# Optimization experiments

Hardware: AMD Instinct MI355X
Metric: run time of the kernel (lower is better)

## Reference

```python
import jax, jax.numpy as jnp
import numpy as np

N_VERTS = 100000  # vertices per mesh; K = 3*N_VERTS


def det3x3(m):
    # m: [..., 3, 3] closed-form determinant (cheaper than generic LU det)
    a00, a01, a02 = m[..., 0, 0], m[..., 0, 1], m[..., 0, 2]
    a10, a11, a12 = m[..., 1, 0], m[..., 1, 1], m[..., 1, 2]
    a20, a21, a22 = m[..., 2, 0], m[..., 2, 1], m[..., 2, 2]
    return (a00 * (a11 * a22 - a12 * a21)
            - a01 * (a10 * a22 - a12 * a20)
            + a02 * (a10 * a21 - a11 * a20))


def setup_inputs() -> dict:
    key = jax.random.key(0)
    k1, k2 = jax.random.split(key)
    x = jax.random.normal(k1, (64, 3 * N_VERTS), dtype=jnp.float32)
    M = jax.random.randint(k2, (200000, 3), 0, N_VERTS, dtype=jnp.int64)
    return {"x": x, "M": M}


def reference(x, M):
    B = x.shape[0]
    v = x.reshape(B, -1, 3)          # [B, N, 3]
    tets = v[:, M]                    # gather -> [B, T, 3, 3]
    vol = jnp.sum(jnp.abs(det3x3(tets)), axis=1) / 6.0  # [B]
    scale = vol ** (1.0 / 3.0)        # cube root of volume
    out = v / scale[:, None, None]    # broadcast divide
    return out.reshape(x.shape)
```

## Files before the change

### kernel.cpp

```cpp
#include <hip/hip_runtime.h>
#include <hip/hip_fp16.h>


constexpr int NV   = 100000;
constexpr int NT   = 200000;
constexpr int NB   = 64;
constexpr int ROW  = 3 * NV;
constexpr int ROW4 = ROW / 4;

typedef float vfloat4 __attribute__((ext_vector_type(4)));

__global__ __launch_bounds__(256) void transpose_kernel(
    const float* __restrict__ x, __half* __restrict__ xt, float* __restrict__ ws)
{
    __shared__ float tile[64][65];
    if (blockIdx.x == 0 && threadIdx.x < NB) ws[threadIdx.x] = 0.0f;

    const int c0 = blockIdx.x * 64;
    const int l  = threadIdx.x & 63;
    const int w  = threadIdx.x >> 6;

    const int c = c0 + l;
    if (c < ROW) {
        #pragma unroll
        for (int k = 0; k < 16; ++k) {
            const int b = w * 16 + k;
            tile[l][b] = x[(size_t)b * ROW + c];
        }
    }
    __syncthreads();

    const int b2 = (l & 31) * 2;
    #pragma unroll
    for (int k = 0; k < 8; ++k) {
        const int r  = (l >> 5) + 2 * w + 8 * k;
        const int cc = c0 + r;
        if (cc < ROW) {
            __half2 h = __floats2half2_rn(tile[r][b2], tile[r][b2 + 1]);
            *(__half2*)&xt[(size_t)cc * NB + b2] = h;
        }
    }
}

__global__ __launch_bounds__(256) void vol_reduce_kernel(
    const __half* __restrict__ xt,
    const int*    __restrict__ M,
    float*        __restrict__ ws)
{
    const int lane  = threadIdx.x & 63;
    const int wib   = threadIdx.x >> 6;
    const int wid   = blockIdx.x * 4 + wib;
    const int nw    = gridDim.x * 4;
    const int chunk = (NT + nw - 1) / nw;
    const int t0 = wid * chunk;
    const int t1 = min(NT, t0 + chunk);

    const __half* __restrict__ base = xt + lane;
    float acc = 0.0f;
    #pragma unroll 4
    for (int t = t0; t < t1; ++t) {
        const int i0 = M[3 * t + 0];
        const int i1 = M[3 * t + 1];
        const int i2 = M[3 * t + 2];
        const __half* p0 = base + (size_t)i0 * 192;
        const __half* p1 = base + (size_t)i1 * 192;
        const __half* p2 = base + (size_t)i2 * 192;
        const float a00 = __half2float(p0[0]);
        const float a01 = __half2float(p0[64]);
        const float a02 = __half2float(p0[128]);
        const float a10 = __half2float(p1[0]);
        const float a11 = __half2float(p1[64]);
        const float a12 = __half2float(p1[128]);
        const float a20 = __half2float(p2[0]);
        const float a21 = __half2float(p2[64]);
        const float a22 = __half2float(p2[128]);
        const float det = a00 * (a11 * a22 - a12 * a21)
                        - a01 * (a10 * a22 - a12 * a20)
                        + a02 * (a10 * a21 - a11 * a20);
        acc += fabsf(det);
    }

    __shared__ float sacc[4][NB];
    sacc[wib][lane] = acc;
    __syncthreads();
    if (threadIdx.x < NB)
        atomicAdd(&ws[threadIdx.x],
                  sacc[0][threadIdx.x] + sacc[1][threadIdx.x] +
                  sacc[2][threadIdx.x] + sacc[3][threadIdx.x]);
}

__global__ __launch_bounds__(256) void scale_kernel(
    const vfloat4* __restrict__ x,
    const float*   __restrict__ ws,
    vfloat4*       __restrict__ out)
{
    const int idx = blockIdx.x * 256 + threadIdx.x;
    const int b   = idx / ROW4;
    const float s = cbrtf(6.0f / ws[b]);
    vfloat4 vv = x[idx];
    vv *= s;
    __builtin_nontemporal_store(vv, &out[idx]);
}

extern "C" void kernel_launch(void* const* d_in, const int* in_sizes, int n_in,
                              void* d_out, int out_size, void* d_ws, size_t ws_size,
                              hipStream_t stream)
{
    const float* x   = (const float*)d_in[0];
    const int*   M   = (const int*)d_in[1];
    float*       out = (float*)d_out;
    float*       ws  = (float*)d_ws;
    __half*      xt  = (__half*)(ws + 256);

    transpose_kernel<<<(ROW + 63) / 64, 256, 0, stream>>>(x, xt, ws);

    vol_reduce_kernel<<<2048, 256, 0, stream>>>(xt, M, ws);

    scale_kernel<<<NB * ROW4 / 256, 256, 0, stream>>>((const vfloat4*)x, ws, (vfloat4*)out);
}
```

Baseline: 220.1 us.

## Interleave vertex xyz per batch in fp16 table and gather 12-byte vectors

The transposed fp16 table now stores each vertex as [batch][xyz] instead of [coord][batch], so one 12-byte load brings a vertex's xyz for two batches. The volume kernel splits each wave into two halves that handle two tetrahedra, and each lane handles two batches. This replaces nine scattered 2-byte gathers with three vector loads. The transpose kernel is reorganised to tile 32 vertices per block, with index div/mod arithmetic to build packed outputs. A cross-half shuffle then combines the partial sums. The cost is more integer arithmetic in the transpose and 12-byte loads that are only 4-byte aligned.

```diff
diff --git a/kernel.cpp b/kernel.cpp
--- a/kernel.cpp
+++ b/kernel.cpp
@@ -9,36 +9,43 @@
 constexpr int ROW4 = ROW / 4;
 
 typedef float vfloat4 __attribute__((ext_vector_type(4)));
+typedef unsigned int uint3v __attribute__((ext_vector_type(3)));
+
+union gpack { uint3v v; __half h[6]; };
 
 __global__ __launch_bounds__(256) void transpose_kernel(
     const float* __restrict__ x, __half* __restrict__ xt, float* __restrict__ ws)
 {
-    __shared__ float tile[64][65];
+    __shared__ float tile[96][65];
     if (blockIdx.x == 0 && threadIdx.x < NB) ws[threadIdx.x] = 0.0f;
 
-    const int c0 = blockIdx.x * 64;
-    const int l  = threadIdx.x & 63;
-    const int w  = threadIdx.x >> 6;
+    const int v0 = blockIdx.x * 32;
+    const int c0 = v0 * 3;
 
-    const int c = c0 + l;
-    if (c < ROW) {
-        #pragma unroll
-        for (int k = 0; k < 16; ++k) {
-            const int b = w * 16 + k;
-            tile[l][b] = x[(size_t)b * ROW + c];
-        }
+    #pragma unroll
+    for (int k = 0; k < 24; ++k) {
+        const int idx = threadIdx.x + k * 256;
+        const int b   = idx / 96;
+        const int cc  = idx - b * 96;
+        tile[cc][b] = x[(size_t)b * ROW + c0 + cc];
     }
     __syncthreads();
 
-    const int b2 = (l & 31) * 2;
+    uint2* outp = (uint2*)(xt + (size_t)v0 * 192);
     #pragma unroll
-    for (int k = 0; k < 8; ++k) {
-        const int r  = (l >> 5) + 2 * w + 8 * k;
-        const int cc = c0 + r;
-        if (cc < ROW) {
-            __half2 h = __floats2half2_rn(tile[r][b2], tile[r][b2 + 1]);
-            *(__half2*)&xt[(size_t)cc * NB + b2] = h;
+    for (int k = 0; k < 6; ++k) {
+        const int j = threadIdx.x + k * 256;
+        union { uint2 u; __half h[4]; } pk;
+        #pragma unroll
+        for (int i = 0; i < 4; ++i) {
+            const int o   = 4 * j + i;
+            const int dv  = o / 192;
+            const int rem = o - dv * 192;
+            const int b   = rem / 3;
+            const int c   = rem - b * 3;
+            pk.h[i] = __float2half_rn(tile[3 * dv + c][b]);
         }
+        outp[j] = pk.u;
     }
 }
 
@@ -47,41 +54,56 @@
     const int*    __restrict__ M,
     float*        __restrict__ ws)
 {
-    const int lane  = threadIdx.x & 63;
-    const int wib   = threadIdx.x >> 6;
-    const int wid   = blockIdx.x * 4 + wib;
-    const int nw    = gridDim.x * 4;
-    const int chunk = (NT + nw - 1) / nw;
-    const int t0 = wid * chunk;
-    const int t1 = min(NT, t0 + chunk);
+    const int lane = threadIdx.x & 63;
+    const int wib  = threadIdx.x >> 6;
+    const int wid  = blockIdx.x * 4 + wib;
+    const int nw   = gridDim.x * 4;
+    const int NP   = NT / 2;
+    const int chunk = (NP + nw - 1) / nw;
+    const int p0 = wid * chunk;
+    const int p1 = min(NP, p0 + chunk);
 
-    const __half* __restrict__ base = xt + lane;
-    float acc = 0.0f;
+    const int hsel = lane >> 5;
+    const int bl   = lane & 31;
+    const __half* __restrict__ base = xt + bl * 6;
+
+    float accA = 0.0f, accB = 0.0f;
     #pragma unroll 4
-    for (int t = t0; t < t1; ++t) {
-        const int i0 = M[3 * t + 0];
-        const int i1 = M[3 * t + 1];
-        const int i2 = M[3 * t + 2];
-        const __half* p0 = base + (size_t)i0 * 192;
-        const __half* p1 = base + (size_t)i1 * 192;
-        const __half* p2 = base + (size_t)i2 * 192;
-        const float a00 = __half2float(p0[0]);
-        const float a01 = __half2float(p0[64]);
-        const float a02 = __half2float(p0[128]);
-        const float a10 = __half2float(p1[0]);
-        const float a11 = __half2float(p1[64]);
-        const float a12 = __half2float(p1[128]);
-        const float a20 = __half2float(p2[0]);
-        const float a21 = __half2float(p2[64]);
-        const float a22 = __half2float(p2[128]);
-        const float det = a00 * (a11 * a22 - a12 * a21)
-                        - a01 * (a10 * a22 - a12 * a20)
-                        + a02 * (a10 * a21 - a11 * a20);
-        acc += fabsf(det);
+    for (int p = p0; p < p1; ++p) {
+        const int t = 2 * p + hsel;
+        const uint3v mi = *(const uint3v*)(M + 3 * t);
+
+        gpack g0, g1, g2;
+        g0.v = *(const uint3v*)(base + (size_t)mi.x * 192);
+        g1.v = *(const uint3v*)(base + (size_t)mi.y * 192);
+        g2.v = *(const uint3v*)(base + (size_t)mi.z * 192);
+
+        {
+            const float a00=__half2float(g0.h[0]), a01=__half2float(g0.h[1]), a02=__half2float(g0.h[2]);
+            const float a10=__half2float(g1.h[0]), a11=__half2float(g1.h[1]), a12=__half2float(g1.h[2]);
+            const float a20=__half2float(g2.h[0]), a21=__half2float(g2.h[1]), a22=__half2float(g2.h[2]);
+            accA += fabsf(a00*(a11*a22 - a12*a21)
+                        - a01*(a10*a22 - a12*a20)
+                        + a02*(a10*a21 - a11*a20));
+        }
+        {
+            const float a00=__half2float(g0.h[3]), a01=__half2float(g0.h[4]), a02=__half2float(g0.h[5]);
+            const float a10=__half2float(g1.h[3]), a11=__half2float(g1.h[4]), a12=__half2float(g1.h[5]);
+            const float a20=__half2float(g2.h[3]), a21=__half2float(g2.h[4]), a22=__half2float(g2.h[5]);
+            accB += fabsf(a00*(a11*a22 - a12*a21)
+                        - a01*(a10*a22 - a12*a20)
+                        + a02*(a10*a21 - a11*a20));
+        }
     }
 
+    accA += __shfl_xor(accA, 32);
+    accB += __shfl_xor(accB, 32);
+
     __shared__ float sacc[4][NB];
-    sacc[wib][lane] = acc;
+    if (lane < 32) {
+        sacc[wib][2 * bl]     = accA;
+        sacc[wib][2 * bl + 1] = accB;
+    }
     __syncthreads();
     if (threadIdx.x < NB)
         atomicAdd(&ws[threadIdx.x],
@@ -112,7 +134,7 @@
     float*       ws  = (float*)d_ws;
     __half*      xt  = (__half*)(ws + 256);
 
-    transpose_kernel<<<(ROW + 63) / 64, 256, 0, stream>>>(x, xt, ws);
+    transpose_kernel<<<NV / 32, 256, 0, stream>>>(x, xt, ws);
 
     vol_reduce_kernel<<<2048, 256, 0, stream>>>(xt, M, ws);
 
```

Measured after the change: 228.7 us. 3.9% more time.
